# Performance work log

Hardware: AMD Instinct MI355X
Metric: run time of the kernel (lower is better)

## Reference

```python
import jax, jax.numpy as jnp
import numpy as np

B, T, D = 4, 4096, 1024


def setup_inputs() -> dict:
    key = jax.random.key(0)
    ks = jax.random.split(key, 7)
    s_in = 1.0 / np.sqrt(D)
    return {
        "x": jax.random.normal(ks[0], (B, T, D), dtype=jnp.float32),
        "W_in": jax.random.uniform(ks[1], (D, 2 * D), jnp.float32, -s_in, s_in),
        "b_in": jax.random.uniform(ks[2], (2 * D,), jnp.float32, -s_in, s_in),
        "A": jax.random.normal(ks[3], (D,), dtype=jnp.float32),
        "C": jax.random.normal(ks[4], (D,), dtype=jnp.float32),
        "W_out": jax.random.uniform(ks[5], (D, D), jnp.float32, -s_in, s_in),
        "b_out": jax.random.uniform(ks[6], (D,), jnp.float32, -s_in, s_in),
    }


def _ssm(v, A, C):
    # diagonal linear recurrence: h_t = sigmoid(A) * h_{t-1} + v_t ; y_t = C * h_t
    decay = jax.nn.sigmoid(A)  # (D,)
    vT = jnp.swapaxes(v, 0, 1)  # (T, B, D)

    def step(h, vt):
        h = decay * h + vt
        return h, h

    h0 = jnp.zeros(vT.shape[1:], dtype=v.dtype)
    _, hs = jax.lax.scan(step, h0, vT)  # (T, B, D)
    return jnp.swapaxes(hs, 0, 1) * C  # (B, T, D)


def reference(x, W_in, b_in, A, C, W_out, b_out):
    proj = x @ W_in + b_in  # (B, T, 2D)
    v, gate = jnp.split(proj, 2, axis=-1)
    gate = jax.nn.sigmoid(gate)
    y = gate * _ssm(v, A, C)
    return y @ W_out + b_out
```

## Files before the change

### kernel.cpp

```cpp
#include <hip/hip_runtime.h>
#include <math.h>

#define BDIM 4
#define TDIM 4096
#define DDIM 1024
#define MDIM (BDIM * TDIM)

#define NC  64
#define LCH 64
static_assert(NC * LCH == TDIM, "chunking");

typedef __attribute__((ext_vector_type(8))) short short8;
typedef __attribute__((ext_vector_type(4))) float f32x4;

__device__ __forceinline__ unsigned short f2bf(float f) {
  unsigned int u = __float_as_uint(f);
  unsigned int r = (u + 0x7fffu + ((u >> 16) & 1u)) >> 16;
  return (unsigned short)r;
}
__device__ __forceinline__ float bf2f(unsigned short h) {
  return __uint_as_float(((unsigned int)h) << 16);
}
__device__ __forceinline__ float sigmoidf_(float x) {
  return 1.0f / (1.0f + expf(-x));
}

__global__ __launch_bounds__(256) void prep_x_kernel(const float* __restrict__ x,
                                                     unsigned short* __restrict__ xh,
                                                     int n4) {
  int i = blockIdx.x * 256 + threadIdx.x;
  if (i >= n4) return;
  float4 f = ((const float4*)x)[i];
  ushort4 h;
  h.x = f2bf(f.x);
  h.y = f2bf(f.y);
  h.z = f2bf(f.z);
  h.w = f2bf(f.w);
  ((ushort4*)xh)[i] = h;
}

__global__ __launch_bounds__(256) void wprep_kernel(const float* __restrict__ in,
                                                    unsigned short* __restrict__ oh,
                                                    int K, int N) {
  __shared__ float t[64][65];
  int n0 = blockIdx.x * 64;
  int k0 = blockIdx.y * 64;
#pragma unroll
  for (int i = 0; i < 16; ++i) {
    int idx = i * 256 + threadIdx.x;
    int r = idx >> 6, c = idx & 63;
    t[r][c] = in[(size_t)(k0 + r) * N + (n0 + c)];
  }
  __syncthreads();
#pragma unroll
  for (int i = 0; i < 16; ++i) {
    int idx = i * 256 + threadIdx.x;
    int rn = idx >> 6, ck = idx & 63;
    oh[(size_t)(n0 + rn) * K + (k0 + ck)] = f2bf(t[ck][rn]);
  }
}


__device__ __forceinline__ void stage_tile(unsigned short* ldsTile,
                                           const unsigned short* __restrict__ gTile,
                                           int ldK) {
  int wave = threadIdx.x >> 6;
  int lane = threadIdx.x & 63;
#pragma unroll
  for (int half = 0; half < 2; ++half) {
#pragma unroll
    for (int j = 0; j < 2; ++j) {
      int c = wave * 64 + lane + j * 512;
      int Lt = half * 16384 + c * 16;
      int P = Lt ^ (((Lt >> 7) & 7) << 4);
      const unsigned short* src = gTile + (size_t)(P >> 7) * ldK + ((P & 127) >> 1);
      unsigned short* dst = ldsTile + (half * 16384 + wave * 1024 + j * 8192) / 2;
      __builtin_amdgcn_global_load_lds(
          (const __attribute__((address_space(1))) unsigned int*)src,
          (__attribute__((address_space(3))) unsigned int*)dst, 16, 0, 0);
    }
  }
}

__device__ __forceinline__ short8 read_frag(const unsigned short* tile, int r, int kElem) {
  int addr = ((r << 7) + (kElem << 1)) ^ ((r & 7) << 4);
  return *(const short8*)((const char*)tile + addr);
}

#define GEMM_PHASE(KK, H, STAGECODE, TAILCODE)                                  \
  {                                                                             \
    short8 af[4];                                                               \
    _Pragma("unroll") for (int m = 0; m < 4; ++m)                               \
        af[m] = read_frag(As, rA + (H) * 64 + m * 16, (KK) * 32 + kq);          \
    if ((H) == 0) {                                                             \
      _Pragma("unroll") for (int n = 0; n < 4; ++n)                             \
          bfr[n] = read_frag(Bs, rB + n * 16, (KK) * 32 + kq);                  \
    }                                                                           \
    STAGECODE                                                                   \
    asm volatile("" ::: "memory");                                              \
    __builtin_amdgcn_s_barrier();                                               \
    asm volatile("" ::: "memory");                                              \
    __builtin_amdgcn_s_setprio(1);                                              \
    _Pragma("unroll") for (int m = 0; m < 4; ++m)                               \
        _Pragma("unroll") for (int n = 0; n < 4; ++n)                           \
            acc[(H) * 4 + m][n] = __builtin_amdgcn_mfma_f32_16x16x32_bf16(      \
                af[m], bfr[n], acc[(H) * 4 + m][n], 0, 0, 0);                   \
    __builtin_amdgcn_s_setprio(0);                                              \
    TAILCODE                                                                    \
    asm volatile("" ::: "memory");                                              \
    __builtin_amdgcn_s_barrier();                                               \
  }

template <int EPI>
__global__ __launch_bounds__(512, 2) void gemm8p(const unsigned short* __restrict__ A,
                                                 const unsigned short* __restrict__ B,
                                                 const float* __restrict__ bias,
                                                 float* __restrict__ outF,
                                                 unsigned short* __restrict__ outG,
                                                 int nNt, int K) {
  __shared__ unsigned short ldsA[2 * 16384];
  __shared__ unsigned short ldsB[2 * 16384];

  int cpx = gridDim.x >> 3;
  int bid = blockIdx.x;
  int swz = (bid & 7) * cpx + (bid >> 3);
  int mtile = swz / nNt, ntile = swz % nNt;

  int wave = threadIdx.x >> 6, lane = threadIdx.x & 63;
  int wm = wave >> 2, wn = wave & 3;
  int rA = wm * 128 + (lane & 15);
  int rB = wn * 64 + (lane & 15);
  int kq = (lane >> 4) * 8;

  const unsigned short* Ag = A + (size_t)(mtile * 256) * K;
  const unsigned short* Bg = B + (size_t)(ntile * 256) * K;

  f32x4 acc[8][4] = {};
  short8 bfr[4];

  stage_tile(ldsA, Ag, K);
  stage_tile(ldsB, Bg, K);
  asm volatile("s_waitcnt vmcnt(0)" ::: "memory");
  __builtin_amdgcn_s_barrier();
  asm volatile("" ::: "memory");

  int NT = K >> 6;
  for (int t = 0; t < NT; ++t) {
    const unsigned short* As = ldsA + (t & 1) * 16384;
    const unsigned short* Bs = ldsB + (t & 1) * 16384;
    unsigned short* An = ldsA + ((t + 1) & 1) * 16384;
    unsigned short* Bn = ldsB + ((t + 1) & 1) * 16384;
    bool pf = (t + 1 < NT);
    int k1 = (t + 1) << 6;

    GEMM_PHASE(0, 0, { if (pf) stage_tile(An, Ag + k1, K); }, {})
    GEMM_PHASE(0, 1, { if (pf) stage_tile(Bn, Bg + k1, K); }, {})
    GEMM_PHASE(1, 0, {}, {})
    GEMM_PHASE(1, 1, {}, {
      if (pf) asm volatile("s_waitcnt vmcnt(0)" ::: "memory");
    })
  }

  int row0 = mtile * 256 + wm * 128 + ((lane >> 4) << 2);
  int col0 = ntile * 256 + wn * 64 + (lane & 15);
#pragma unroll
  for (int m = 0; m < 8; ++m) {
#pragma unroll
    for (int n = 0; n < 4; ++n) {
      int col = col0 + n * 16;
      float bv = bias[col];
#pragma unroll
      for (int j = 0; j < 4; ++j) {
        int row = row0 + m * 16 + j;
        float val = acc[m][n][j] + bv;
        if (EPI == 0) {
          outF[(size_t)row * (nNt * 256) + col] = val;
        } else {
          if (col < DDIM)
            outF[(size_t)row * DDIM + col] = val;
          else
            outG[(size_t)row * DDIM + (col - DDIM)] = f2bf(sigmoidf_(val));
        }
      }
    }
  }
}

__global__ __launch_bounds__(256) void ssm_phase1(const float* __restrict__ v,
                                                  const float* __restrict__ A,
                                                  float* __restrict__ chunkh) {
  int b = blockIdx.y, c = blockIdx.x;
  int d0 = threadIdx.x * 4;
  float4 a4 = *(const float4*)&A[d0];
  float dx = sigmoidf_(a4.x), dy = sigmoidf_(a4.y), dz = sigmoidf_(a4.z), dw = sigmoidf_(a4.w);
  float hx = 0.f, hy = 0.f, hz = 0.f, hw = 0.f;
  const float4* vp = (const float4*)(v + ((size_t)b * TDIM + (size_t)c * LCH) * DDIM + d0);
#pragma unroll 4
  for (int i = 0; i < LCH; ++i) {
    float4 vv = vp[(size_t)i * (DDIM / 4)];
    hx = fmaf(dx, hx, vv.x);
    hy = fmaf(dy, hy, vv.y);
    hz = fmaf(dz, hz, vv.z);
    hw = fmaf(dw, hw, vv.w);
  }
  float4 o = {hx, hy, hz, hw};
  *(float4*)&chunkh[(size_t)(b * NC + c) * DDIM + d0] = o;
}

__global__ __launch_bounds__(256) void ssm_phase2(const float* __restrict__ A,
                                                  float* __restrict__ chunkh) {
  int idx = blockIdx.x * 256 + threadIdx.x;
  int b = idx >> 10, d = idx & 1023;
  float dec = sigmoidf_(A[d]);
  float dL = dec;
#pragma unroll
  for (int i = 0; i < 6; ++i) dL *= dL;
  float hv[NC];
#pragma unroll
  for (int c = 0; c < NC; ++c) hv[c] = chunkh[(size_t)(b * NC + c) * DDIM + d];
  float carry = 0.f;
#pragma unroll
  for (int c = 0; c < NC; ++c) {
    float local = hv[c];
    hv[c] = carry;
    carry = fmaf(dL, carry, local);
  }
#pragma unroll
  for (int c = 0; c < NC; ++c) chunkh[(size_t)(b * NC + c) * DDIM + d] = hv[c];
}

__global__ __launch_bounds__(256) void ssm_phase3(const float* __restrict__ v,
                                                  const unsigned short* __restrict__ g,
                                                  const float* __restrict__ A,
                                                  const float* __restrict__ C,
                                                  const float* __restrict__ chunkh,
                                                  unsigned short* __restrict__ ybf) {
  int b = blockIdx.y, c = blockIdx.x;
  int d0 = threadIdx.x * 4;
  float4 a4 = *(const float4*)&A[d0];
  float4 c4 = *(const float4*)&C[d0];
  float dx = sigmoidf_(a4.x), dy = sigmoidf_(a4.y), dz = sigmoidf_(a4.z), dw = sigmoidf_(a4.w);
  float4 h0 = *(const float4*)&chunkh[(size_t)(b * NC + c) * DDIM + d0];
  float hx = h0.x, hy = h0.y, hz = h0.z, hw = h0.w;
  size_t base = ((size_t)b * TDIM + (size_t)c * LCH) * DDIM + d0;
  const float4* vp = (const float4*)(v + base);
  const ushort4* gp = (const ushort4*)(g + base);
  ushort4* yp = (ushort4*)(ybf + base);
#pragma unroll 4
  for (int i = 0; i < LCH; ++i) {
    float4 vv = vp[(size_t)i * (DDIM / 4)];
    ushort4 gg = gp[(size_t)i * (DDIM / 4)];
    hx = fmaf(dx, hx, vv.x);
    hy = fmaf(dy, hy, vv.y);
    hz = fmaf(dz, hz, vv.z);
    hw = fmaf(dw, hw, vv.w);
    ushort4 yy;
    yy.x = f2bf(bf2f(gg.x) * c4.x * hx);
    yy.y = f2bf(bf2f(gg.y) * c4.y * hy);
    yy.z = f2bf(bf2f(gg.z) * c4.z * hz);
    yy.w = f2bf(bf2f(gg.w) * c4.w * hw);
    yp[(size_t)i * (DDIM / 4)] = yy;
  }
}

extern "C" void kernel_launch(void* const* d_in, const int* in_sizes, int n_in,
                              void* d_out, int out_size, void* d_ws, size_t ws_size,
                              hipStream_t stream) {
  const float* x = (const float*)d_in[0];
  const float* W_in = (const float*)d_in[1];
  const float* b_in = (const float*)d_in[2];
  const float* A = (const float*)d_in[3];
  const float* C = (const float*)d_in[4];
  const float* W_out = (const float*)d_in[5];
  const float* b_out = (const float*)d_in[6];
  float* out = (float*)d_out;

  char* ws = (char*)d_ws;
  const size_t MK = (size_t)MDIM * DDIM;
  unsigned short* xh = (unsigned short*)ws;    ws += MK * 2;
  unsigned short* winh = (unsigned short*)ws;  ws += (size_t)2 * DDIM * DDIM * 2;
  unsigned short* wouth = (unsigned short*)ws; ws += (size_t)DDIM * DDIM * 2;
  float* v = (float*)ws;                       ws += MK * 4;
  unsigned short* g = (unsigned short*)ws;     ws += MK * 2;
  unsigned short* ybf = (unsigned short*)ws;   ws += MK * 2;
  float* chunkh = (float*)ws;                  ws += (size_t)BDIM * NC * DDIM * 4;

  prep_x_kernel<<<(int)(MK / 4 / 256), 256, 0, stream>>>(x, xh, (int)(MK / 4));
  wprep_kernel<<<dim3(2 * DDIM / 64, DDIM / 64), 256, 0, stream>>>(W_in, winh, DDIM, 2 * DDIM);
  wprep_kernel<<<dim3(DDIM / 64, DDIM / 64), 256, 0, stream>>>(W_out, wouth, DDIM, DDIM);

  gemm8p<1><<<(MDIM / 256) * 8, 512, 0, stream>>>(xh, winh, b_in, v, g, 8, DDIM);

  ssm_phase1<<<dim3(NC, BDIM), 256, 0, stream>>>(v, A, chunkh);
  ssm_phase2<<<(BDIM * DDIM) / 256, 256, 0, stream>>>(A, chunkh);
  ssm_phase3<<<dim3(NC, BDIM), 256, 0, stream>>>(v, g, A, C, chunkh, ybf);

  gemm8p<0><<<(MDIM / 256) * 4, 512, 0, stream>>>(ybf, wouth, b_out, out, nullptr, 4, DDIM);
}
```

Measured before the change: 204.0 us.

## Double-buffer A fragments across GEMM phases and store v as bf16

The GEMM inner loop is restructured so the A-fragment LDS reads for the next half-tile are issued before the barrier and overlap the current MFMA block, using two fragment register sets. Separately, the v projection is written as bf16 instead of fp32, halving its write traffic and the reads in the two SSM scan kernels. The interleaving adds register pressure, and bf16 v adds rounding error to the recurrence input.

```diff
diff --git a/kernel.cpp b/kernel.cpp
--- a/kernel.cpp
+++ b/kernel.cpp
@@ -87,35 +87,35 @@
   return *(const short8*)((const char*)tile + addr);
 }
 
-#define GEMM_PHASE(KK, H, STAGECODE, TAILCODE)                                  \
-  {                                                                             \
-    short8 af[4];                                                               \
-    _Pragma("unroll") for (int m = 0; m < 4; ++m)                               \
-        af[m] = read_frag(As, rA + (H) * 64 + m * 16, (KK) * 32 + kq);          \
-    if ((H) == 0) {                                                             \
+#define BARRIER()                                  \
+  do {                                             \
+    asm volatile("" ::: "memory");                 \
+    __builtin_amdgcn_s_barrier();                  \
+    asm volatile("" ::: "memory");                 \
+  } while (0)
+
+#define READ_AF(SET, H, KKv)                                                    \
+  _Pragma("unroll") for (int m = 0; m < 4; ++m)                                 \
+      SET[m] = read_frag(As, rA + (H) * 64 + m * 16, (KKv) * 32 + kq);
+
+#define READ_BF(KKv)                                                            \
+  _Pragma("unroll") for (int n = 0; n < 4; ++n)                                 \
+      bfr[n] = read_frag(Bs, rB + n * 16, (KKv) * 32 + kq);
+
+#define MFMA16(SET, HH)                                                         \
+  __builtin_amdgcn_s_setprio(1);                                                \
+  _Pragma("unroll") for (int m = 0; m < 4; ++m)                                 \
       _Pragma("unroll") for (int n = 0; n < 4; ++n)                             \
-          bfr[n] = read_frag(Bs, rB + n * 16, (KK) * 32 + kq);                  \
-    }                                                                           \
-    STAGECODE                                                                   \
-    asm volatile("" ::: "memory");                                              \
-    __builtin_amdgcn_s_barrier();                                               \
-    asm volatile("" ::: "memory");                                              \
-    __builtin_amdgcn_s_setprio(1);                                              \
-    _Pragma("unroll") for (int m = 0; m < 4; ++m)                               \
-        _Pragma("unroll") for (int n = 0; n < 4; ++n)                           \
-            acc[(H) * 4 + m][n] = __builtin_amdgcn_mfma_f32_16x16x32_bf16(      \
-                af[m], bfr[n], acc[(H) * 4 + m][n], 0, 0, 0);                   \
-    __builtin_amdgcn_s_setprio(0);                                              \
-    TAILCODE                                                                    \
-    asm volatile("" ::: "memory");                                              \
-    __builtin_amdgcn_s_barrier();                                               \
-  }
+          acc[(HH) * 4 + m][n] = __builtin_amdgcn_mfma_f32_16x16x32_bf16(       \
+              SET[m], bfr[n], acc[(HH) * 4 + m][n], 0, 0, 0);                   \
+  __builtin_amdgcn_s_setprio(0);
 
 template <int EPI>
 __global__ __launch_bounds__(512, 2) void gemm8p(const unsigned short* __restrict__ A,
                                                  const unsigned short* __restrict__ B,
                                                  const float* __restrict__ bias,
                                                  float* __restrict__ outF,
+                                                 unsigned short* __restrict__ outV,
                                                  unsigned short* __restrict__ outG,
                                                  int nNt, int K) {
   __shared__ unsigned short ldsA[2 * 16384];
@@ -136,13 +136,12 @@
   const unsigned short* Bg = B + (size_t)(ntile * 256) * K;
 
   f32x4 acc[8][4] = {};
-  short8 bfr[4];
+  short8 afA[4], afB[4], bfr[4];
 
   stage_tile(ldsA, Ag, K);
   stage_tile(ldsB, Bg, K);
   asm volatile("s_waitcnt vmcnt(0)" ::: "memory");
-  __builtin_amdgcn_s_barrier();
-  asm volatile("" ::: "memory");
+  BARRIER();
 
   int NT = K >> 6;
   for (int t = 0; t < NT; ++t) {
@@ -153,12 +152,23 @@
     bool pf = (t + 1 < NT);
     int k1 = (t + 1) << 6;
 
-    GEMM_PHASE(0, 0, { if (pf) stage_tile(An, Ag + k1, K); }, {})
-    GEMM_PHASE(0, 1, { if (pf) stage_tile(Bn, Bg + k1, K); }, {})
-    GEMM_PHASE(1, 0, {}, {})
-    GEMM_PHASE(1, 1, {}, {
-      if (pf) asm volatile("s_waitcnt vmcnt(0)" ::: "memory");
-    })
+    READ_AF(afA, 0, 0);
+    READ_BF(0);
+    MFMA16(afA, 0);
+    READ_AF(afB, 1, 0);
+    if (pf) stage_tile(An, Ag + k1, K);
+    BARRIER();
+    MFMA16(afB, 1);
+    READ_AF(afA, 0, 1);
+    READ_BF(1);
+    if (pf) stage_tile(Bn, Bg + k1, K);
+    BARRIER();
+    MFMA16(afA, 0);
+    READ_AF(afB, 1, 1);
+    BARRIER();
+    MFMA16(afB, 1);
+    if (pf) asm volatile("s_waitcnt vmcnt(0)" ::: "memory");
+    BARRIER();
   }
 
   int row0 = mtile * 256 + wm * 128 + ((lane >> 4) << 2);
@@ -177,7 +187,7 @@
           outF[(size_t)row * (nNt * 256) + col] = val;
         } else {
           if (col < DDIM)
-            outF[(size_t)row * DDIM + col] = val;
+            outV[(size_t)row * DDIM + col] = f2bf(val);
           else
             outG[(size_t)row * DDIM + (col - DDIM)] = f2bf(sigmoidf_(val));
         }
@@ -186,7 +196,7 @@
   }
 }
 
-__global__ __launch_bounds__(256) void ssm_phase1(const float* __restrict__ v,
+__global__ __launch_bounds__(256) void ssm_phase1(const unsigned short* __restrict__ v,
                                                   const float* __restrict__ A,
                                                   float* __restrict__ chunkh) {
   int b = blockIdx.y, c = blockIdx.x;
@@ -194,14 +204,14 @@
   float4 a4 = *(const float4*)&A[d0];
   float dx = sigmoidf_(a4.x), dy = sigmoidf_(a4.y), dz = sigmoidf_(a4.z), dw = sigmoidf_(a4.w);
   float hx = 0.f, hy = 0.f, hz = 0.f, hw = 0.f;
-  const float4* vp = (const float4*)(v + ((size_t)b * TDIM + (size_t)c * LCH) * DDIM + d0);
+  const ushort4* vp = (const ushort4*)(v + ((size_t)b * TDIM + (size_t)c * LCH) * DDIM + d0);
 #pragma unroll 4
   for (int i = 0; i < LCH; ++i) {
-    float4 vv = vp[(size_t)i * (DDIM / 4)];
-    hx = fmaf(dx, hx, vv.x);
-    hy = fmaf(dy, hy, vv.y);
-    hz = fmaf(dz, hz, vv.z);
-    hw = fmaf(dw, hw, vv.w);
+    ushort4 vv = vp[(size_t)i * (DDIM / 4)];
+    hx = fmaf(dx, hx, bf2f(vv.x));
+    hy = fmaf(dy, hy, bf2f(vv.y));
+    hz = fmaf(dz, hz, bf2f(vv.z));
+    hw = fmaf(dw, hw, bf2f(vv.w));
   }
   float4 o = {hx, hy, hz, hw};
   *(float4*)&chunkh[(size_t)(b * NC + c) * DDIM + d0] = o;
@@ -229,7 +239,7 @@
   for (int c = 0; c < NC; ++c) chunkh[(size_t)(b * NC + c) * DDIM + d] = hv[c];
 }
 
-__global__ __launch_bounds__(256) void ssm_phase3(const float* __restrict__ v,
+__global__ __launch_bounds__(256) void ssm_phase3(const unsigned short* __restrict__ v,
                                                   const unsigned short* __restrict__ g,
                                                   const float* __restrict__ A,
                                                   const float* __restrict__ C,
@@ -243,17 +253,17 @@
   float4 h0 = *(const float4*)&chunkh[(size_t)(b * NC + c) * DDIM + d0];
   float hx = h0.x, hy = h0.y, hz = h0.z, hw = h0.w;
   size_t base = ((size_t)b * TDIM + (size_t)c * LCH) * DDIM + d0;
-  const float4* vp = (const float4*)(v + base);
+  const ushort4* vp = (const ushort4*)(v + base);
   const ushort4* gp = (const ushort4*)(g + base);
   ushort4* yp = (ushort4*)(ybf + base);
 #pragma unroll 4
   for (int i = 0; i < LCH; ++i) {
-    float4 vv = vp[(size_t)i * (DDIM / 4)];
+    ushort4 vv = vp[(size_t)i * (DDIM / 4)];
     ushort4 gg = gp[(size_t)i * (DDIM / 4)];
-    hx = fmaf(dx, hx, vv.x);
-    hy = fmaf(dy, hy, vv.y);
-    hz = fmaf(dz, hz, vv.z);
-    hw = fmaf(dw, hw, vv.w);
+    hx = fmaf(dx, hx, bf2f(vv.x));
+    hy = fmaf(dy, hy, bf2f(vv.y));
+    hz = fmaf(dz, hz, bf2f(vv.z));
+    hw = fmaf(dw, hw, bf2f(vv.w));
     ushort4 yy;
     yy.x = f2bf(bf2f(gg.x) * c4.x * hx);
     yy.y = f2bf(bf2f(gg.y) * c4.y * hy);
@@ -280,7 +290,7 @@
   unsigned short* xh = (unsigned short*)ws;    ws += MK * 2;
   unsigned short* winh = (unsigned short*)ws;  ws += (size_t)2 * DDIM * DDIM * 2;
   unsigned short* wouth = (unsigned short*)ws; ws += (size_t)DDIM * DDIM * 2;
-  float* v = (float*)ws;                       ws += MK * 4;
+  unsigned short* v = (unsigned short*)ws;     ws += MK * 2;
   unsigned short* g = (unsigned short*)ws;     ws += MK * 2;
   unsigned short* ybf = (unsigned short*)ws;   ws += MK * 2;
   float* chunkh = (float*)ws;                  ws += (size_t)BDIM * NC * DDIM * 4;
@@ -289,11 +299,12 @@
   wprep_kernel<<<dim3(2 * DDIM / 64, DDIM / 64), 256, 0, stream>>>(W_in, winh, DDIM, 2 * DDIM);
   wprep_kernel<<<dim3(DDIM / 64, DDIM / 64), 256, 0, stream>>>(W_out, wouth, DDIM, DDIM);
 
-  gemm8p<1><<<(MDIM / 256) * 8, 512, 0, stream>>>(xh, winh, b_in, v, g, 8, DDIM);
+  gemm8p<1><<<(MDIM / 256) * 8, 512, 0, stream>>>(xh, winh, b_in, nullptr, v, g, 8, DDIM);
 
   ssm_phase1<<<dim3(NC, BDIM), 256, 0, stream>>>(v, A, chunkh);
   ssm_phase2<<<(BDIM * DDIM) / 256, 256, 0, stream>>>(A, chunkh);
   ssm_phase3<<<dim3(NC, BDIM), 256, 0, stream>>>(v, g, A, C, chunkh, ybf);
 
-  gemm8p<0><<<(MDIM / 256) * 4, 512, 0, stream>>>(ybf, wouth, b_out, out, nullptr, 4, DDIM);
-}
+  gemm8p<0><<<(MDIM / 256) * 4, 512, 0, stream>>>(ybf, wouth, b_out, out, nullptr, nullptr,
+                                                  4, DDIM);
+}
```

Result: faster. 186.6 us (-8.5%).
